# Kernel optimization log

Hardware: AMD Instinct MI355X
Metric: run time of the kernel (lower is better)

The kernel has to match this reference:

```python
import jax, jax.numpy as jnp
import numpy as np
import math

B, SEQ, D, E = 8, 2049, 1024, 8
H = 4 * D // E  # 512
MULT = 4
MAX_SEQ = 2048

def _capacity(n, e, cf=1.0, mult=MULT):
    cap = max(math.ceil(n * cf / e), 1)
    r = cap % mult
    if r != 0:
        cap += mult - r
    return cap

MAX_SLOTS = _capacity(MAX_SEQ, E)  # 256

def setup_inputs() -> dict:
    key = jax.random.key(0)
    ks = jax.random.split(key, 12)
    std_mu = math.sqrt(1.0 / (E * MAX_SLOTS))  # kaiming fan_in on [D,E,slots]
    return {
        "x": jax.random.normal(ks[0], (B, SEQ, D), jnp.float32),
        "mu": jax.random.normal(ks[1], (D, E, MAX_SLOTS), jnp.float32) * std_mu,
        "scale": jnp.ones((1,), jnp.float32),
        "cls_w1": jax.random.normal(ks[2], (H, D), jnp.float32) * math.sqrt(2.0 / D),
        "cls_b1": jnp.zeros((H,), jnp.float32),
        "cls_w2": jax.random.normal(ks[3], (D, H), jnp.float32) * math.sqrt(2.0 / H),
        "cls_b2": jnp.zeros((D,), jnp.float32),
        "w1": jax.random.normal(ks[4], (E, H, D), jnp.float32) * math.sqrt(2.0 / D),
        "b1": jnp.zeros((E, H), jnp.float32),
        "w2": jax.random.normal(ks[5], (E, D, H), jnp.float32) * math.sqrt(2.0 / (D + H)),
        "b2": jnp.zeros((E, D), jnp.float32),
    }

def _gelu(v):
    return jax.nn.gelu(v, approximate=False)

def _metrics(combine, dispatch):
    # exact scalar values of the source's cosine_psim metrics, computed without
    # materializing the rank-4/5 outer-product similarity tensors.
    b, n, e, s = combine.shape
    es = e * s
    # combine: normalize over (E,S), flatten to [B,N,ES]
    tn = combine * jax.lax.rsqrt(jnp.sum(combine * combine, axis=(2, 3), keepdims=True) + 1e-9)
    tnf = tn.reshape(b, n, es)
    r = tnf.sum(-1)                       # [B,N] row sums
    sum_total = jnp.sum(r * r)            # sum over [B,N,ES,ES] outer products
    k = min(n, es)
    idx = jnp.arange(k)
    diag_vals = tnf[:, idx, idx]          # A[b,k,k,:] factor
    sum_diag = jnp.sum(diag_vals * r[:, :k])
    m1 = (sum_total - sum_diag) / (b * n * (n - 1))
    # dispatch: permute to [B,E,S,N], normalize over N
    y = jnp.transpose(dispatch, (0, 2, 3, 1))
    yn = y * jax.lax.rsqrt(jnp.sum(y * y, axis=3, keepdims=True) + 1e-9)
    rs = yn.sum(-1)                       # [B,E,S]
    st = jnp.sum(rs * rs)
    k2 = min(e, s)
    i2 = jnp.arange(k2)
    sd = jnp.sum(rs[:, i2, i2] ** 2)
    m2 = (st - sd) / (b * e * s * (es - 1))
    return m1, m2

def reference(x, mu, scale, cls_w1, cls_b1, cls_w2, cls_b2, w1, b1, w2, b2):
    cls_tok = x[:, 0, :]
    cls_emd = _gelu(cls_tok @ cls_w1.T + cls_b1) @ cls_w2.T + cls_b2
    cls_emd = cls_emd[:, None, :]                        # [B,1,D]
    xt = x[:, 1:, :]
    b, n, d = xt.shape
    e = E
    s = _capacity(n, e)
    mu_s = mu[:, :, :s]                                  # [D,E,S]
    x_norm = xt / jnp.maximum(jnp.linalg.norm(xt, axis=-1, keepdims=True), 1e-12)
    mu_norm = mu_s / jnp.maximum(jnp.linalg.norm(mu_s, axis=0, keepdims=True), 1e-12)
    if xt.size < mu_s.size:
        x_norm = x_norm * scale
    else:
        mu_norm = mu_norm * scale
    logits = jnp.einsum('bnd,des->bnes', x_norm, mu_norm)        # [B,N,E,S]
    dispatch = jax.nn.softmax(logits, axis=1)                    # over tokens
    combine_flat = jax.nn.softmax(logits.reshape(b, n, e * s), axis=-1)
    combine = combine_flat.reshape(b, n, e, s)
    slot_in = jnp.einsum('bnd,bnes->besd', xt, dispatch)         # [B,E,S,D]
    # per-expert MLP as batched (grouped) GEMM
    h = _gelu(jnp.einsum('besd,ehd->besh', slot_in, w1) + b1[:, None, :])
    slot_out = jnp.einsum('besh,edh->besd', h, w2) + b2[:, None, :]
    flat = slot_out.reshape(b, e * s, d)
    img = jnp.einsum('bsd,bns->bnd', flat, combine_flat)
    outputs = jnp.concatenate([cls_emd, img], axis=1)            # [B,N+1,D]
    m1, m2 = _metrics(combine, dispatch)
    return outputs, m1, m2
```

## Files before the change

kernel.cpp:

```cpp
#include <hip/hip_runtime.h>
#include <math.h>

#define BB 8
#define SEQ 2049
#define NT 2048
#define DD 1024
#define EE 8
#define SS 256
#define ESN 2048
#define HH 512

typedef __bf16 bf16x8 __attribute__((ext_vector_type(8)));
typedef float f32x4 __attribute__((ext_vector_type(4)));

__device__ __forceinline__ float gelu_f(float v) {
  return 0.5f * v * (1.0f + erff(v * 0.70710678118654752440f));
}
__device__ __forceinline__ float wave_sum(float v) {
#pragma unroll
  for (int off = 1; off < 64; off <<= 1) v += __shfl_xor(v, off);
  return v;
}
__device__ __forceinline__ unsigned short f2bf(float f) {
  unsigned int u = __float_as_uint(f);
  u = (u + 0x7fffu + ((u >> 16) & 1u)) >> 16;
  return (unsigned short)u;
}
__device__ __forceinline__ float bf2f(unsigned short h) {
  return __uint_as_float(((unsigned int)h) << 16);
}

__device__ __forceinline__ void stage16(const unsigned short* g, unsigned short* lbase, int lane) {
#if __has_builtin(__builtin_amdgcn_global_load_lds)
  __builtin_amdgcn_global_load_lds((const __attribute__((address_space(1))) void*)g,
                                   (__attribute__((address_space(3))) void*)lbase, 16, 0, 0);
#else
  *(int4*)(lbase + lane * 8) = *(const int4*)g;
#endif
}

__device__ __forceinline__ int3 xcd_map() {
  const int gx = gridDim.x, gy = gridDim.y;
  int bid = blockIdx.x + gx * (blockIdx.y + gy * blockIdx.z);
  const int q = (gx * gy * (int)gridDim.z) >> 3;
  bid = (bid & 7) * q + (bid >> 3);
  int3 r;
  r.x = bid % gx; bid /= gx;
  r.y = bid % gy;
  r.z = bid / gy;
  return r;
}

__device__ __forceinline__ void gemm_core(const unsigned short* __restrict__ A,
                                          const unsigned short* __restrict__ B,
                                          int K, unsigned short* LDS, f32x4 acc[4][4]) {
  const int t = threadIdx.x;
  const int lane = t & 63, wave = t >> 6;
  const int srow = t >> 3, scol = (t & 7) * 8;
  const int fr = lane & 15, fk = (lane >> 4) * 8;
  const int wm = (wave >> 1) * 64, wn = (wave & 1) * 64;
  const unsigned short* ap = A + (size_t)srow * K + scol;
  const unsigned short* bp = B + (size_t)srow * K + scol;
  unsigned short* dA = LDS + wave * 512;
  unsigned short* dB = LDS + 8192 + wave * 512;
  for (int k0 = 0; k0 < K; k0 += 64) {
#pragma unroll
    for (int q = 0; q < 4; ++q) {
      stage16(ap + (size_t)(q * 32) * K + k0, dA + q * 2048, lane);
      stage16(bp + (size_t)(q * 32) * K + k0, dB + q * 2048, lane);
    }
    __syncthreads();
#pragma unroll
    for (int kk = 0; kk < 2; ++kk) {
      bf16x8 bq[4];
#pragma unroll
      for (int j = 0; j < 4; ++j)
        bq[j] = *(const bf16x8*)(LDS + 8192 + (wn + j * 16 + fr) * 64 + kk * 32 + fk);
#pragma unroll
      for (int ib = 0; ib < 2; ++ib) {
        bf16x8 afa = *(const bf16x8*)(LDS + (wm + (ib * 2) * 16 + fr) * 64 + kk * 32 + fk);
        bf16x8 afb = *(const bf16x8*)(LDS + (wm + (ib * 2 + 1) * 16 + fr) * 64 + kk * 32 + fk);
#pragma unroll
        for (int j = 0; j < 4; ++j)
          acc[ib * 2][j] = __builtin_amdgcn_mfma_f32_16x16x32_bf16(afa, bq[j], acc[ib * 2][j], 0, 0, 0);
#pragma unroll
        for (int j = 0; j < 4; ++j)
          acc[ib * 2 + 1][j] = __builtin_amdgcn_mfma_f32_16x16x32_bf16(afb, bq[j], acc[ib * 2 + 1][j], 0, 0, 0);
      }
    }
    __syncthreads();
  }
}

#define ACC_INIT()                                        \
  f32x4 acc[4][4];                                        \
  _Pragma("unroll") for (int i = 0; i < 4; ++i)           \
  _Pragma("unroll") for (int j = 0; j < 4; ++j)           \
  _Pragma("unroll") for (int r = 0; r < 4; ++r) acc[i][j][r] = 0.f;

#define GEMM_EPI_VARS()                                   \
  const int lane = threadIdx.x & 63, wave = threadIdx.x >> 6; \
  const int wm = (wave >> 1) * 64, wn = (wave & 1) * 64;  \
  const int fr16 = lane & 15, r4 = (lane >> 4) << 2;

__global__ __launch_bounds__(256, 4) void k_logits_mfma(const unsigned short* __restrict__ Xb,
    const unsigned short* __restrict__ MT, unsigned short* __restrict__ E16,
    unsigned short* __restrict__ ET) {
  __shared__ unsigned short LDS[16384];
  ACC_INIT();
  const int3 bi = xcd_map();
  const int b = bi.z, m0 = bi.x * 128, n0 = bi.y * 128;
  gemm_core(Xb + ((size_t)b * NT + m0) * DD, MT + (size_t)n0 * DD, DD, LDS, acc);
  GEMM_EPI_VARS();
  const int t = threadIdx.x;
  unsigned short* o = E16 + (size_t)b * NT * ESN;
#pragma unroll
  for (int i = 0; i < 4; ++i)
#pragma unroll
    for (int j = 0; j < 4; ++j) {
      const int gmb = m0 + wm + i * 16 + r4;
      const int gn = n0 + wn + j * 16 + fr16;
      o[(size_t)(gmb + 0) * ESN + gn] = f2bf(expf(acc[i][j][0]));
      o[(size_t)(gmb + 1) * ESN + gn] = f2bf(expf(acc[i][j][1]));
      o[(size_t)(gmb + 2) * ESN + gn] = f2bf(expf(acc[i][j][2]));
      o[(size_t)(gmb + 3) * ESN + gn] = f2bf(expf(acc[i][j][3]));
    }
#pragma unroll
  for (int h = 0; h < 2; ++h) {
    if ((wn >> 6) == h) {
#pragma unroll
      for (int i = 0; i < 4; ++i)
#pragma unroll
        for (int j = 0; j < 4; ++j) {
          ushort4 pk;
          pk.x = f2bf(expf(acc[i][j][0]));
          pk.y = f2bf(expf(acc[i][j][1]));
          pk.z = f2bf(expf(acc[i][j][2]));
          pk.w = f2bf(expf(acc[i][j][3]));
          *(ushort4*)(LDS + (j * 16 + fr16) * 132 + wm + i * 16 + r4) = pk;
        }
    }
    __syncthreads();
#pragma unroll
    for (int p = 0; p < 4; ++p) {
      const int nl = p * 16 + (t >> 4);
      const int ml = (t & 15) * 8;
      int4 v = *(const int4*)(LDS + nl * 132 + ml);
      *(int4*)(ET + ((size_t)b * ESN + n0 + h * 64 + nl) * NT + m0 + ml) = v;
    }
    __syncthreads();
  }
}

__global__ __launch_bounds__(256, 4) void k_slotin_mfma(const unsigned short* __restrict__ ET,
    const unsigned short* __restrict__ XT, const float* __restrict__ cinv,
    unsigned short* __restrict__ SI) {
  __shared__ unsigned short LDS[16384];
  ACC_INIT();
  const int3 bi = xcd_map();
  const int b = bi.z, m0 = bi.x * 128, n0 = bi.y * 128;
  gemm_core(ET + ((size_t)b * ESN + m0) * NT, XT + ((size_t)b * DD + n0) * NT, NT, LDS, acc);
  GEMM_EPI_VARS();
#pragma unroll
  for (int i = 0; i < 4; ++i)
#pragma unroll
    for (int j = 0; j < 4; ++j) {
      const int gmb = m0 + wm + i * 16 + r4;
      const int gn = n0 + wn + j * 16 + fr16;
#pragma unroll
      for (int r = 0; r < 4; ++r)
        SI[((size_t)b * ESN + gmb + r) * DD + gn] = f2bf(acc[i][j][r] * cinv[b * ESN + gmb + r]);
    }
}

__global__ __launch_bounds__(256, 4) void k_ffn1_mfma(const unsigned short* __restrict__ SI,
    const unsigned short* __restrict__ w1b, const float* __restrict__ b1,
    unsigned short* __restrict__ H1) {
  __shared__ unsigned short LDS[16384];
  ACC_INIT();
  const int3 bi = xcd_map();
  const int z = bi.z, b = z >> 3, e = z & 7;
  const int m0 = bi.x * 128, n0 = bi.y * 128;
  gemm_core(SI + ((size_t)b * ESN + e * SS + m0) * DD, w1b + ((size_t)e * HH + n0) * DD,
            DD, LDS, acc);
  GEMM_EPI_VARS();
#pragma unroll
  for (int i = 0; i < 4; ++i)
#pragma unroll
    for (int j = 0; j < 4; ++j) {
      const int gmb = m0 + wm + i * 16 + r4;
      const int gn = n0 + wn + j * 16 + fr16;
      const float bias = b1[e * HH + gn];
#pragma unroll
      for (int r = 0; r < 4; ++r)
        H1[((size_t)(b * EE + e) * SS + gmb + r) * HH + gn] = f2bf(gelu_f(acc[i][j][r] + bias));
    }
}

__global__ __launch_bounds__(256, 4) void k_ffn2_mfma(const unsigned short* __restrict__ H1,
    const unsigned short* __restrict__ w2b, const float* __restrict__ b2,
    unsigned short* __restrict__ SOT) {
  __shared__ unsigned short LDS[16384];
  ACC_INIT();
  const int3 bi = xcd_map();
  const int z = bi.z, b = z >> 3, e = z & 7;
  const int m0 = bi.x * 128, n0 = bi.y * 128;
  gemm_core(H1 + ((size_t)(b * EE + e) * SS + m0) * HH, w2b + ((size_t)e * DD + n0) * HH,
            HH, LDS, acc);
  GEMM_EPI_VARS();
  const int t = threadIdx.x;
#pragma unroll
  for (int h = 0; h < 2; ++h) {
    if ((wn >> 6) == h) {
#pragma unroll
      for (int i = 0; i < 4; ++i)
#pragma unroll
        for (int j = 0; j < 4; ++j) {
          const float bias = b2[e * DD + n0 + wn + j * 16 + fr16];
          ushort4 pk;
          pk.x = f2bf(acc[i][j][0] + bias);
          pk.y = f2bf(acc[i][j][1] + bias);
          pk.z = f2bf(acc[i][j][2] + bias);
          pk.w = f2bf(acc[i][j][3] + bias);
          *(ushort4*)(LDS + (j * 16 + fr16) * 132 + wm + i * 16 + r4) = pk;
        }
    }
    __syncthreads();
#pragma unroll
    for (int p = 0; p < 4; ++p) {
      const int dl = p * 16 + (t >> 4);
      const int ml = (t & 15) * 8;
      int4 v = *(const int4*)(LDS + dl * 132 + ml);
      *(int4*)(SOT + ((size_t)b * DD + n0 + h * 64 + dl) * ESN + e * SS + m0 + ml) = v;
    }
    __syncthreads();
  }
}

__global__ __launch_bounds__(256, 4) void k_img_mfma(const unsigned short* __restrict__ E16,
    const unsigned short* __restrict__ SOT, const float* __restrict__ rinv,
    float* __restrict__ out) {
  __shared__ unsigned short LDS[16384];
  ACC_INIT();
  const int3 bi = xcd_map();
  const int b = bi.z, m0 = bi.x * 128, n0 = bi.y * 128;
  gemm_core(E16 + ((size_t)b * NT + m0) * ESN, SOT + ((size_t)b * DD + n0) * ESN,
            ESN, LDS, acc);
  GEMM_EPI_VARS();
#pragma unroll
  for (int i = 0; i < 4; ++i)
#pragma unroll
    for (int j = 0; j < 4; ++j) {
      const int gmb = m0 + wm + i * 16 + r4;
      const int gn = n0 + wn + j * 16 + fr16;
#pragma unroll
      for (int r = 0; r < 4; ++r)
        out[((size_t)b * SEQ + 1 + gmb + r) * DD + gn] = acc[i][j][r] * rinv[b * NT + gmb + r];
    }
}

__global__ __launch_bounds__(256) void k_xnf(const float* __restrict__ x, float* __restrict__ xnf) {
  const int wid = blockIdx.x * 4 + (threadIdx.x >> 6);
  const int lane = threadIdx.x & 63;
  const int b = wid >> 11;
  const float* row = x + ((size_t)b * SEQ + 1 + (wid & (NT - 1))) * DD;
  float s = 0.f;
#pragma unroll
  for (int k = 0; k < DD / 64; ++k) { const float v = row[lane + k * 64]; s = fmaf(v, v, s); }
  s = wave_sum(s);
  if (lane == 0) xnf[wid] = 1.0f / fmaxf(sqrtf(s), 1e-12f);
}

__global__ __launch_bounds__(256) void k_munf_part(const float* __restrict__ mu,
    float* __restrict__ pm) {
  const int c = blockIdx.x * 256 + threadIdx.x;
  const int d0 = blockIdx.y * (DD / 16);
  float s = 0.f;
  for (int d = d0; d < d0 + DD / 16; ++d) {
    const float v = mu[(size_t)d * ESN + c];
    s = fmaf(v, v, s);
  }
  pm[blockIdx.y * ESN + c] = s;
}

__global__ __launch_bounds__(256) void k_munf_red(const float* __restrict__ pm,
    const float* __restrict__ scale, float* __restrict__ munf) {
  const int c = blockIdx.x * 256 + threadIdx.x;
  float s = 0.f;
#pragma unroll
  for (int k = 0; k < 16; ++k) s += pm[k * ESN + c];
  munf[c] = scale[0] / fmaxf(sqrtf(s), 1e-12f);
}

__global__ __launch_bounds__(256) void k_pack_x(const float* __restrict__ x,
    const float* __restrict__ xnf, unsigned short* __restrict__ Xb,
    unsigned short* __restrict__ XT) {
  __shared__ unsigned short tile[64][72];
  const int b = blockIdx.z, n0 = blockIdx.x * 64, d0 = blockIdx.y * 64;
  const int t = threadIdx.x, tr = t >> 2, tc = (t & 3) * 16;
  const float* s = x + ((size_t)b * SEQ + 1 + n0 + tr) * DD + d0 + tc;
  const float xs = xnf[b * NT + n0 + tr];
  unsigned short tmp[16];
#pragma unroll
  for (int j = 0; j < 16; j += 4) {
    float4 v = *(const float4*)(s + j);
    tmp[j] = f2bf(v.x * xs); tmp[j + 1] = f2bf(v.y * xs);
    tmp[j + 2] = f2bf(v.z * xs); tmp[j + 3] = f2bf(v.w * xs);
  }
  *(int4*)&tile[tr][tc] = *(int4*)tmp;
  *(int4*)&tile[tr][tc + 8] = *(int4*)(tmp + 8);
  unsigned short* xb = Xb + ((size_t)b * NT + n0 + tr) * DD + d0 + tc;
  *(int4*)xb = *(int4*)tmp;
  *(int4*)(xb + 8) = *(int4*)(tmp + 8);
  __syncthreads();
  unsigned short* d = XT + ((size_t)b * DD + d0 + tr) * NT + n0 + tc;
#pragma unroll
  for (int j = 0; j < 16; ++j) tmp[j] = tile[tc + j][tr];
  *(int4*)d = *(int4*)tmp;
  *(int4*)(d + 8) = *(int4*)(tmp + 8);
}

__global__ __launch_bounds__(256) void k_pack_mu(const float* __restrict__ mu,
    const float* __restrict__ munf, unsigned short* __restrict__ MT) {
  __shared__ unsigned short tile[64][72];
  const int d0 = blockIdx.x * 64, c0 = blockIdx.y * 64;
  const int t = threadIdx.x, tr = t >> 2, tc = (t & 3) * 16;
  const float* s = mu + (size_t)(d0 + tr) * ESN + c0 + tc;
  unsigned short tmp[16];
#pragma unroll
  for (int j = 0; j < 16; j += 4) {
    float4 v = *(const float4*)(s + j);
    tmp[j] = f2bf(v.x * munf[c0 + tc + j]);
    tmp[j + 1] = f2bf(v.y * munf[c0 + tc + j + 1]);
    tmp[j + 2] = f2bf(v.z * munf[c0 + tc + j + 2]);
    tmp[j + 3] = f2bf(v.w * munf[c0 + tc + j + 3]);
  }
  *(int4*)&tile[tr][tc] = *(int4*)tmp;
  *(int4*)&tile[tr][tc + 8] = *(int4*)(tmp + 8);
  __syncthreads();
  unsigned short* d = MT + (size_t)(c0 + tr) * DD + d0 + tc;
#pragma unroll
  for (int j = 0; j < 16; ++j) tmp[j] = tile[tc + j][tr];
  *(int4*)d = *(int4*)tmp;
  *(int4*)(d + 8) = *(int4*)(tmp + 8);
}

__global__ __launch_bounds__(256) void k_packw(const float* __restrict__ w,
    unsigned short* __restrict__ o, int n4) {
  const int i = blockIdx.x * 256 + threadIdx.x;
  if (i < n4) {
    float4 v = ((const float4*)w)[i];
    ushort4 u;
    u.x = f2bf(v.x); u.y = f2bf(v.y); u.z = f2bf(v.z); u.w = f2bf(v.w);
    ((ushort4*)o)[i] = u;
  }
}

__global__ __launch_bounds__(256) void k_rowstats_e(const unsigned short* __restrict__ E,
    float* __restrict__ rinv, float* __restrict__ t_r2, float* __restrict__ t_dr) {
  const int wid = blockIdx.x * 4 + (threadIdx.x >> 6);
  const int lane = threadIdx.x & 63;
  const int n = wid & (NT - 1);
  const unsigned short* row = E + (size_t)wid * ESN;
  float s1 = 0.f, s2 = 0.f;
#pragma unroll
  for (int it = 0; it < 4; ++it) {
    int4 v = *(const int4*)(row + it * 512 + lane * 8);
    const unsigned short* u = (const unsigned short*)&v;
#pragma unroll
    for (int j = 0; j < 8; ++j) { const float e = bf2f(u[j]); s1 += e; s2 = fmaf(e, e, s2); }
  }
  s1 = wave_sum(s1); s2 = wave_sum(s2);
  if (lane == 0) {
    const float ri = 1.0f / s1;
    rinv[wid] = ri;
    const float r2 = 1.0f / (s2 * ri * ri + 1e-9f);
    t_r2[wid] = r2;
    t_dr[wid] = bf2f(row[n]) * ri * r2;
  }
}

__global__ __launch_bounds__(256) void k_colstats(const unsigned short* __restrict__ ET,
    float* __restrict__ cinv, float* __restrict__ t_rs2, float* __restrict__ t_sd) {
  const int wid = blockIdx.x * 4 + (threadIdx.x >> 6);
  const int lane = threadIdx.x & 63;
  const unsigned short* row = ET + (size_t)wid * NT;
  float s1 = 0.f, s2 = 0.f;
#pragma unroll
  for (int it = 0; it < 4; ++it) {
    int4 v = *(const int4*)(row + it * 512 + lane * 8);
    const unsigned short* u = (const unsigned short*)&v;
#pragma unroll
    for (int j = 0; j < 8; ++j) { const float e = bf2f(u[j]); s1 += e; s2 = fmaf(e, e, s2); }
  }
  s1 = wave_sum(s1); s2 = wave_sum(s2);
  if (lane == 0) {
    const float ci = 1.0f / s1;
    cinv[wid] = ci;
    const float rs2 = 1.0f / (s2 * ci * ci + 1e-9f);
    t_rs2[wid] = rs2;
    const int c = wid & (ESN - 1);
    t_sd[wid] = ((c % 257) == 0) ? rs2 : 0.f;
  }
}

__global__ __launch_bounds__(256) void k_clsA(const float* __restrict__ x,
    const float* __restrict__ w1, const float* __restrict__ b1, float* __restrict__ clsh) {
  const int wid = blockIdx.x * 4 + (threadIdx.x >> 6);
  const int lane = threadIdx.x & 63;
  const int b = wid >> 9, h = wid & (HH - 1);
  const float* xr = x + (size_t)b * SEQ * DD;
  const float* wr = w1 + (size_t)h * DD;
  float s = 0.f;
#pragma unroll
  for (int k = 0; k < DD / 64; ++k) s = fmaf(xr[lane + k * 64], wr[lane + k * 64], s);
  s = wave_sum(s);
  if (lane == 0) clsh[wid] = gelu_f(s + b1[h]);
}

__global__ __launch_bounds__(256) void k_clsB(const float* __restrict__ clsh,
    const float* __restrict__ w2, const float* __restrict__ b2, float* __restrict__ out) {
  const int wid = blockIdx.x * 4 + (threadIdx.x >> 6);
  const int lane = threadIdx.x & 63;
  const int b = wid >> 10, d = wid & (DD - 1);
  const float* hr = clsh + (size_t)b * HH;
  const float* wr = w2 + (size_t)d * HH;
  float s = 0.f;
#pragma unroll
  for (int k = 0; k < HH / 64; ++k) s = fmaf(hr[lane + k * 64], wr[lane + k * 64], s);
  s = wave_sum(s);
  if (lane == 0) out[(size_t)b * SEQ * DD + d] = s + b2[d];
}

__global__ __launch_bounds__(256) void k_metrics(const float* __restrict__ t_r2,
    const float* __restrict__ t_dr, const float* __restrict__ t_rs2,
    const float* __restrict__ t_sd, float* __restrict__ out) {
  __shared__ float sm[256];
  const int tid = threadIdx.x;
  float a = 0.f, b = 0.f, c = 0.f, d = 0.f;
  for (int i = tid; i < BB * NT; i += 256) { a += t_r2[i]; b += t_dr[i]; }
  for (int i = tid; i < BB * ESN; i += 256) { c += t_rs2[i]; d += t_sd[i]; }
  float vals[4] = {a, b, c, d};
  float res[4];
#pragma unroll
  for (int v = 0; v < 4; ++v) {
    sm[tid] = vals[v];
    __syncthreads();
    for (int s = 128; s > 0; s >>= 1) {
      if (tid < s) sm[tid] += sm[tid + s];
      __syncthreads();
    }
    res[v] = sm[0];
    __syncthreads();
  }
  if (tid == 0) {
    out[(size_t)BB * SEQ * DD] = (res[0] - res[1]) / 33538048.0f;
    out[(size_t)BB * SEQ * DD + 1] = (res[2] - res[3]) / 33538048.0f;
  }
}

extern "C" void kernel_launch(void* const* d_in, const int* in_sizes, int n_in,
                              void* d_out, int out_size, void* d_ws, size_t ws_size,
                              hipStream_t stream) {
  const float* x      = (const float*)d_in[0];
  const float* mu     = (const float*)d_in[1];
  const float* scale  = (const float*)d_in[2];
  const float* cls_w1 = (const float*)d_in[3];
  const float* cls_b1 = (const float*)d_in[4];
  const float* cls_w2 = (const float*)d_in[5];
  const float* cls_b2 = (const float*)d_in[6];
  const float* w1     = (const float*)d_in[7];
  const float* b1     = (const float*)d_in[8];
  const float* w2     = (const float*)d_in[9];
  const float* b2     = (const float*)d_in[10];
  float* out = (float*)d_out;

  char* W = (char*)d_ws;
  unsigned short* XT  = (unsigned short*)(W);
  unsigned short* Xb  = (unsigned short*)(W + 33554432);
  unsigned short* MT  = (unsigned short*)(W + 67108864);
  unsigned short* E16 = (unsigned short*)(W + 71303168);
  unsigned short* ET  = (unsigned short*)(W + 138412032);
  unsigned short* SI  = (unsigned short*)(W + 205520896);
  unsigned short* H1  = (unsigned short*)(W);
  unsigned short* SOT = (unsigned short*)(W + 33554432);
  unsigned short* w1b = (unsigned short*)(W + 138412032);
  unsigned short* w2b = (unsigned short*)(W + 146800640);
  float* pmunf = (float*)(W + 71303168);
  float* F = (float*)(W + 239075328);
  float* xnf   = F;
  float* munf  = F + 16384;
  float* rinv  = F + 18432;
  float* t_r2  = F + 34816;
  float* t_dr  = F + 51200;
  float* cinv  = F + 67584;
  float* t_rs2 = F + 83968;
  float* t_sd  = F + 100352;
  float* clsh  = F + 116736;

  k_xnf<<<dim3(BB * NT / 4), 256, 0, stream>>>(x, xnf);
  k_munf_part<<<dim3(ESN / 256, 16), 256, 0, stream>>>(mu, pmunf);
  k_munf_red<<<dim3(ESN / 256), 256, 0, stream>>>(pmunf, scale, munf);
  k_pack_x<<<dim3(NT / 64, DD / 64, BB), 256, 0, stream>>>(x, xnf, Xb, XT);
  k_pack_mu<<<dim3(DD / 64, ESN / 64), 256, 0, stream>>>(mu, munf, MT);
  k_logits_mfma<<<dim3(NT / 128, ESN / 128, BB), 256, 0, stream>>>(Xb, MT, E16, ET);
  k_rowstats_e<<<dim3(BB * NT / 4), 256, 0, stream>>>(E16, rinv, t_r2, t_dr);
  k_colstats<<<dim3(BB * ESN / 4), 256, 0, stream>>>(ET, cinv, t_rs2, t_sd);
  k_slotin_mfma<<<dim3(ESN / 128, DD / 128, BB), 256, 0, stream>>>(ET, XT, cinv, SI);
  k_packw<<<dim3(EE * HH * DD / 4 / 256), 256, 0, stream>>>(w1, w1b, EE * HH * DD / 4);
  k_packw<<<dim3(EE * DD * HH / 4 / 256), 256, 0, stream>>>(w2, w2b, EE * DD * HH / 4);
  k_ffn1_mfma<<<dim3(SS / 128, HH / 128, BB * EE), 256, 0, stream>>>(SI, w1b, b1, H1);
  k_ffn2_mfma<<<dim3(SS / 128, DD / 128, BB * EE), 256, 0, stream>>>(H1, w2b, b2, SOT);
  k_img_mfma<<<dim3(NT / 128, DD / 128, BB), 256, 0, stream>>>(E16, SOT, rinv, out);
  k_clsA<<<dim3(BB * HH / 4), 256, 0, stream>>>(x, cls_w1, cls_b1, clsh);
  k_clsB<<<dim3(BB * DD / 4), 256, 0, stream>>>(clsh, cls_w2, cls_b2, out);
  k_metrics<<<1, 256, 0, stream>>>(t_r2, t_dr, t_rs2, t_sd, out);
}
```

Before: 447.2 us.

## Double-buffer GEMM LDS staging with XOR swizzle and split waitcnt

Restructures the shared GEMM core from a single 64-wide K tile with full syncthreads into two 32-wide K buffers. The next tile's global-to-LDS loads are issued while the current one is computed, gated by an explicit vmcnt wait and raw barriers. It also applies an XOR swizzle to the LDS column layout to reduce bank conflicts on fragment reads. The risk is correctness of the manual vmcnt counting, since it assumes exactly four outstanding loads per stage, plus more barriers per K step.

```diff
diff --git a/kernel.cpp b/kernel.cpp
--- a/kernel.cpp
+++ b/kernel.cpp
@@ -51,45 +51,64 @@
   return r;
 }
 
+#define MEMFENCE() asm volatile("" ::: "memory")
+
 __device__ __forceinline__ void gemm_core(const unsigned short* __restrict__ A,
                                           const unsigned short* __restrict__ B,
                                           int K, unsigned short* LDS, f32x4 acc[4][4]) {
   const int t = threadIdx.x;
   const int lane = t & 63, wave = t >> 6;
-  const int srow = t >> 3, scol = (t & 7) * 8;
+  const int srow = t >> 2;
+  const int scol = (((t & 3) ^ ((t >> 3) & 3)) << 3);
   const int fr = lane & 15, fk = (lane >> 4) * 8;
+  const int fswz = ((fr >> 1) & 3) << 3;
   const int wm = (wave >> 1) * 64, wn = (wave & 1) * 64;
   const unsigned short* ap = A + (size_t)srow * K + scol;
   const unsigned short* bp = B + (size_t)srow * K + scol;
   unsigned short* dA = LDS + wave * 512;
-  unsigned short* dB = LDS + 8192 + wave * 512;
-  for (int k0 = 0; k0 < K; k0 += 64) {
-#pragma unroll
-    for (int q = 0; q < 4; ++q) {
-      stage16(ap + (size_t)(q * 32) * K + k0, dA + q * 2048, lane);
-      stage16(bp + (size_t)(q * 32) * K + k0, dB + q * 2048, lane);
-    }
-    __syncthreads();
-#pragma unroll
-    for (int kk = 0; kk < 2; ++kk) {
-      bf16x8 bq[4];
+  unsigned short* dB = LDS + 4096 + wave * 512;
+
+  auto STAGE = [&](int pb, int k0) {
+    stage16(ap + k0, dA + pb, lane);
+    stage16(ap + (size_t)64 * K + k0, dA + pb + 2048, lane);
+    stage16(bp + k0, dB + pb, lane);
+    stage16(bp + (size_t)64 * K + k0, dB + pb + 2048, lane);
+  };
+  auto COMPUTE = [&](int pb) {
+    bf16x8 bq[4];
+#pragma unroll
+    for (int j = 0; j < 4; ++j)
+      bq[j] = *(const bf16x8*)(LDS + pb + 4096 + (wn + j * 16 + fr) * 32 + (fk ^ fswz));
+#pragma unroll
+    for (int ib = 0; ib < 2; ++ib) {
+      bf16x8 afa = *(const bf16x8*)(LDS + pb + (wm + ib * 32 + fr) * 32 + (fk ^ fswz));
+      bf16x8 afb = *(const bf16x8*)(LDS + pb + (wm + ib * 32 + 16 + fr) * 32 + (fk ^ fswz));
 #pragma unroll
       for (int j = 0; j < 4; ++j)
-        bq[j] = *(const bf16x8*)(LDS + 8192 + (wn + j * 16 + fr) * 64 + kk * 32 + fk);
-#pragma unroll
-      for (int ib = 0; ib < 2; ++ib) {
-        bf16x8 afa = *(const bf16x8*)(LDS + (wm + (ib * 2) * 16 + fr) * 64 + kk * 32 + fk);
-        bf16x8 afb = *(const bf16x8*)(LDS + (wm + (ib * 2 + 1) * 16 + fr) * 64 + kk * 32 + fk);
-#pragma unroll
-        for (int j = 0; j < 4; ++j)
-          acc[ib * 2][j] = __builtin_amdgcn_mfma_f32_16x16x32_bf16(afa, bq[j], acc[ib * 2][j], 0, 0, 0);
-#pragma unroll
-        for (int j = 0; j < 4; ++j)
-          acc[ib * 2 + 1][j] = __builtin_amdgcn_mfma_f32_16x16x32_bf16(afb, bq[j], acc[ib * 2 + 1][j], 0, 0, 0);
-      }
-    }
-    __syncthreads();
-  }
+        acc[ib * 2][j] = __builtin_amdgcn_mfma_f32_16x16x32_bf16(afa, bq[j], acc[ib * 2][j], 0, 0, 0);
+#pragma unroll
+      for (int j = 0; j < 4; ++j)
+        acc[ib * 2 + 1][j] = __builtin_amdgcn_mfma_f32_16x16x32_bf16(afb, bq[j], acc[ib * 2 + 1][j], 0, 0, 0);
+    }
+  };
+
+  const int nt = K >> 5;
+  STAGE(0, 0);
+  STAGE(8192, 32);
+  for (int tt = 0; tt < nt - 1; ++tt) {
+    asm volatile("s_waitcnt vmcnt(4)" ::: "memory");
+    __builtin_amdgcn_s_barrier();
+    MEMFENCE();
+    COMPUTE((tt & 1) * 8192);
+    MEMFENCE();
+    __builtin_amdgcn_s_barrier();
+    if (tt + 2 < nt) STAGE((tt & 1) * 8192, (tt + 2) << 5);
+  }
+  asm volatile("s_waitcnt vmcnt(0)" ::: "memory");
+  __builtin_amdgcn_s_barrier();
+  MEMFENCE();
+  COMPUTE(((nt - 1) & 1) * 8192);
+  __syncthreads();
 }
 
 #define ACC_INIT()                                        \
```

Result: slower. 470.2 us (+5.2%).
